# Performance work log

Measured on AMD Instinct MI355X. Metric: run time of the kernel, lower is better.

The kernel has to match this reference:

```python
import jax, jax.numpy as jnp
import numpy as np

D_IN, D_HID, D_OUT = 4096, 8192, 1000


def setup_inputs() -> dict:
    key = jax.random.key(0)
    ks = jax.random.split(key, 7)
    s1 = 1.0 / np.sqrt(D_IN)
    s2 = 1.0 / np.sqrt(D_HID)
    return {
        "x": jax.random.normal(ks[0], (D_IN,), dtype=jnp.float32),
        "W1": jax.random.normal(ks[1], (D_HID, D_IN), dtype=jnp.float32) * s1,
        "b1": jax.random.normal(ks[2], (D_HID,), dtype=jnp.float32) * 0.01,
        "W2": jax.random.normal(ks[3], (D_HID, D_HID), dtype=jnp.float32) * s2,
        "b2": jax.random.normal(ks[4], (D_HID,), dtype=jnp.float32) * 0.01,
        "W3": jax.random.normal(ks[5], (D_OUT, D_HID), dtype=jnp.float32) * s2,
        "b3": jax.random.normal(ks[6], (D_OUT,), dtype=jnp.float32) * 0.01,
    }


def reference(x, W1, b1, W2, b2, W3, b3):
    # layer 1: matvec + bias + square activation (h_relu is x*x)
    h = W1 @ x + b1
    h = h * h
    # layer 2
    h = W2 @ h + b2
    h = h * h
    # layer 3 (no activation)
    return W3 @ h + b3
```

## Files before the change

### kernel.cpp

```cpp
#include <hip/hip_runtime.h>


__global__ __launch_bounds__(256) void init_bias(
    const float* __restrict__ b1, const float* __restrict__ b2,
    const float* __restrict__ b3,
    float* __restrict__ h1, float* __restrict__ h2, float* __restrict__ out)
{
    const int i = blockIdx.x * 256 + threadIdx.x;
    if (i < 8192)       h1[i] = b1[i];
    else if (i < 16384) h2[i - 8192] = b2[i - 8192];
    else if (i < 17384) out[i - 16384] = b3[i - 16384];
}

template<int K, int RPB, int SQ>
__global__ __launch_bounds__(256) void matvec_atomic(
    const float* __restrict__ W,
    const float* __restrict__ xin,
    float* __restrict__ y)
{
    constexpr int K4     = K / 4;
    constexpr int CHUNKS = K4 / 256;

    __shared__ __align__(16) float sx[K];
    const int tid = threadIdx.x;

    const float4* __restrict__ x4 = (const float4*)xin;
    float4* sx4 = (float4*)sx;
    #pragma unroll
    for (int c = 0; c < CHUNKS; ++c) {
        const int i = c * 256 + tid;
        float4 v = x4[i];
        if (SQ) { v.x *= v.x; v.y *= v.y; v.z *= v.z; v.w *= v.w; }
        sx4[i] = v;
    }
    __syncthreads();

    const int  c0   = blockIdx.x % CHUNKS;
    const long row0 = (long)blockIdx.x * RPB;

    for (int r = 0; r < RPB; ++r) {
        const long row = row0 + r;
        const float4* __restrict__ Wr = (const float4*)(W + row * (long)K);

        float acc = 0.0f;
        #pragma unroll
        for (int j = 0; j < CHUNKS; ++j) {
            int c = c0 + j; if (c >= CHUNKS) c -= CHUNKS;
            const int i = c * 256 + tid;
            const float4 w = Wr[i];
            const float4 v = sx4[i];
            acc += (w.x * v.x + w.y * v.y) + (w.z * v.z + w.w * v.w);
        }

        #pragma unroll
        for (int off = 32; off > 0; off >>= 1)
            acc += __shfl_down(acc, off, 64);
        if ((tid & 63) == 0) atomicAdd(&y[row], acc);
    }
}

extern "C" void kernel_launch(void* const* d_in, const int* in_sizes, int n_in,
                              void* d_out, int out_size, void* d_ws, size_t ws_size,
                              hipStream_t stream) {
    const float* x  = (const float*)d_in[0];
    const float* W1 = (const float*)d_in[1];
    const float* b1 = (const float*)d_in[2];
    const float* W2 = (const float*)d_in[3];
    const float* b2 = (const float*)d_in[4];
    const float* W3 = (const float*)d_in[5];
    const float* b3 = (const float*)d_in[6];
    float* out = (float*)d_out;

    float* h1 = (float*)d_ws;
    float* h2 = h1 + 8192;

    init_bias<<<68, 256, 0, stream>>>(b1, b2, b3, h1, h2, out);

    matvec_atomic<4096, 8, 0><<<1024, 256, 0, stream>>>(W1, x, h1);
    matvec_atomic<8192, 8, 1><<<1024, 256, 0, stream>>>(W2, h1, h2);
    matvec_atomic<8192, 2, 1><<<500, 256, 0, stream>>>(W3, h2, out);
}
```

Before: 467.7 us.

## Drop shared-memory staging; process rows jointly with register accumulators and column splits

Replaces the shared-memory staging of the input vector with direct global (cached) loads that are reused across R rows processed together, so several independent weight loads are in flight per thread. Removes the __syncthreads and the 32KB of shared memory per block, which raises the number of resident blocks. Adds a column-segment split (NSEG) for the last layer so it launches more blocks, at the cost of more atomics. The input vector is now reloaded from L2/L1 by each block instead of once into LDS.

```diff
diff --git a/kernel.cpp b/kernel.cpp
--- a/kernel.cpp
+++ b/kernel.cpp
@@ -12,50 +12,53 @@
     else if (i < 17384) out[i - 16384] = b3[i - 16384];
 }
 
-template<int K, int RPB, int SQ>
-__global__ __launch_bounds__(256) void matvec_atomic(
+template<int LDK, int COLS, int R, int NSEG, int SQ>
+__global__ __launch_bounds__(256) void matvec(
     const float* __restrict__ W,
     const float* __restrict__ xin,
     float* __restrict__ y)
 {
-    constexpr int K4     = K / 4;
-    constexpr int CHUNKS = K4 / 256;
+    constexpr int C4     = COLS / 4;
+    constexpr int CHUNKS = C4 / 256;
+    static_assert(CHUNKS * 256 == C4, "COLS must be multiple of 1024");
 
-    __shared__ __align__(16) float sx[K];
-    const int tid = threadIdx.x;
+    const int tid  = threadIdx.x;
+    const int g    = blockIdx.x / NSEG;
+    const int s    = blockIdx.x - g * NSEG;
+    const int row0 = g * R;
 
-    const float4* __restrict__ x4 = (const float4*)xin;
-    float4* sx4 = (float4*)sx;
+    const float4* __restrict__ x4 = (const float4*)(xin + (size_t)s * COLS);
+    const float4* W4[R];
     #pragma unroll
-    for (int c = 0; c < CHUNKS; ++c) {
-        const int i = c * 256 + tid;
+    for (int r = 0; r < R; ++r)
+        W4[r] = (const float4*)(W + (size_t)(row0 + r) * LDK + (size_t)s * COLS);
+
+    float acc[R];
+    #pragma unroll
+    for (int r = 0; r < R; ++r) acc[r] = 0.0f;
+
+    #pragma unroll
+    for (int j = 0; j < CHUNKS; ++j) {
+        const int i = j * 256 + tid;
         float4 v = x4[i];
         if (SQ) { v.x *= v.x; v.y *= v.y; v.z *= v.z; v.w *= v.w; }
-        sx4[i] = v;
+        #pragma unroll
+        for (int r = 0; r < R; ++r) {
+            const float4 w = W4[r][i];
+            acc[r] += (w.x * v.x + w.y * v.y) + (w.z * v.z + w.w * v.w);
+        }
     }
-    __syncthreads();
 
-    const int  c0   = blockIdx.x % CHUNKS;
-    const long row0 = (long)blockIdx.x * RPB;
-
-    for (int r = 0; r < RPB; ++r) {
-        const long row = row0 + r;
-        const float4* __restrict__ Wr = (const float4*)(W + row * (long)K);
-
-        float acc = 0.0f;
+    #pragma unroll
+    for (int off = 32; off > 0; off >>= 1) {
         #pragma unroll
-        for (int j = 0; j < CHUNKS; ++j) {
-            int c = c0 + j; if (c >= CHUNKS) c -= CHUNKS;
-            const int i = c * 256 + tid;
-            const float4 w = Wr[i];
-            const float4 v = sx4[i];
-            acc += (w.x * v.x + w.y * v.y) + (w.z * v.z + w.w * v.w);
-        }
-
+        for (int r = 0; r < R; ++r)
+            acc[r] += __shfl_down(acc[r], off, 64);
+    }
+    if ((tid & 63) == 0) {
         #pragma unroll
-        for (int off = 32; off > 0; off >>= 1)
-            acc += __shfl_down(acc, off, 64);
-        if ((tid & 63) == 0) atomicAdd(&y[row], acc);
+        for (int r = 0; r < R; ++r)
+            atomicAdd(&y[row0 + r], acc[r]);
     }
 }
 
@@ -76,7 +79,7 @@
 
     init_bias<<<68, 256, 0, stream>>>(b1, b2, b3, h1, h2, out);
 
-    matvec_atomic<4096, 8, 0><<<1024, 256, 0, stream>>>(W1, x, h1);
-    matvec_atomic<8192, 8, 1><<<1024, 256, 0, stream>>>(W2, h1, h2);
-    matvec_atomic<8192, 2, 1><<<500, 256, 0, stream>>>(W3, h2, out);
+    matvec<4096, 4096, 4, 1, 0><<<2048, 256, 0, stream>>>(W1, x, h1);
+    matvec<8192, 8192, 4, 1, 1><<<2048, 256, 0, stream>>>(W2, h1, h2);
+    matvec<8192, 2048, 4, 4, 1><<<1000, 256, 0, stream>>>(W3, h2, out);
 }
```

New measurement: 463.8 us. About the same (-0.8%).

## Use one wave per row with nontemporal loads and fold bias init into layers

Applied to the files above, without the earlier changes.

Replaces the block-per-row-group matvec, which staged x in shared memory and accumulated with atomics, with a one-wavefront-per-row design. Each wave reads its row of W with nontemporal loads and reads x straight from global/L2, then writes the result plus bias directly with no atomics. The separate bias-init kernel is removed: layer 2 also initializes the output with b3, and layer 3 splits K into 8 segments across blocks and combines them with atomics. This cuts launches, LDS staging and syncs and adds parallelism, at the cost of every wave re-reading x from cache.

```diff
diff --git a/kernel.cpp b/kernel.cpp
--- a/kernel.cpp
+++ b/kernel.cpp
@@ -1,62 +1,79 @@
 #include <hip/hip_runtime.h>
 
 
-__global__ __launch_bounds__(256) void init_bias(
-    const float* __restrict__ b1, const float* __restrict__ b2,
+typedef float f32x4 __attribute__((ext_vector_type(4)));
+
+template<int K, int SQ, int INIT_OUT>
+__global__ __launch_bounds__(256) void matvec_rowwave(
+    const float* __restrict__ W,
+    const float* __restrict__ xin,
+    const float* __restrict__ bias,
+    float* __restrict__ y,
     const float* __restrict__ b3,
-    float* __restrict__ h1, float* __restrict__ h2, float* __restrict__ out)
+    float* __restrict__ out)
 {
-    const int i = blockIdx.x * 256 + threadIdx.x;
-    if (i < 8192)       h1[i] = b1[i];
-    else if (i < 16384) h2[i - 8192] = b2[i - 8192];
-    else if (i < 17384) out[i - 16384] = b3[i - 16384];
+    constexpr int ITER = K / 4 / 64;
+    const int tid  = threadIdx.x;
+    const int wave = tid >> 6;
+    const int lane = tid & 63;
+    const int row  = blockIdx.x * 4 + wave;
+
+    const f32x4* __restrict__ W4 = (const f32x4*)(W + (size_t)row * K);
+    const f32x4* __restrict__ x4 = (const f32x4*)xin;
+
+    float acc = 0.0f;
+    #pragma unroll 8
+    for (int j = 0; j < ITER; ++j) {
+        const int i = j * 64 + lane;
+        const f32x4 w = __builtin_nontemporal_load(&W4[i]);
+        f32x4 v = x4[i];
+        if (SQ) v *= v;
+        acc += (w.x * v.x + w.y * v.y) + (w.z * v.z + w.w * v.w);
+    }
+
+    #pragma unroll
+    for (int off = 32; off > 0; off >>= 1)
+        acc += __shfl_down(acc, off, 64);
+    if (lane == 0) y[row] = acc + bias[row];
+
+    if (INIT_OUT && blockIdx.x < 4) {
+        const int i = blockIdx.x * 256 + tid;
+        if (i < 1000) out[i] = b3[i];
+    }
 }
 
-template<int K, int RPB, int SQ>
-__global__ __launch_bounds__(256) void matvec_atomic(
+template<int K, int NSEG>
+__global__ __launch_bounds__(256) void matvec_l3(
     const float* __restrict__ W,
     const float* __restrict__ xin,
-    float* __restrict__ y)
+    float* __restrict__ out)
 {
-    constexpr int K4     = K / 4;
-    constexpr int CHUNKS = K4 / 256;
+    constexpr int COLS = K / NSEG;
+    constexpr int ITER = COLS / 4 / 64;
+    const int tid  = threadIdx.x;
+    const int wave = tid >> 6;
+    const int lane = tid & 63;
+    const int g    = blockIdx.x / NSEG;
+    const int s    = blockIdx.x - g * NSEG;
+    const int row  = g * 4 + wave;
 
-    __shared__ __align__(16) float sx[K];
-    const int tid = threadIdx.x;
+    const f32x4* __restrict__ W4 = (const f32x4*)(W + (size_t)row * K + (size_t)s * COLS);
+    const f32x4* __restrict__ x4 = (const f32x4*)(xin + (size_t)s * COLS);
 
-    const float4* __restrict__ x4 = (const float4*)xin;
-    float4* sx4 = (float4*)sx;
+    float acc = 0.0f;
     #pragma unroll
-    for (int c = 0; c < CHUNKS; ++c) {
-        const int i = c * 256 + tid;
-        float4 v = x4[i];
-        if (SQ) { v.x *= v.x; v.y *= v.y; v.z *= v.z; v.w *= v.w; }
-        sx4[i] = v;
+    for (int j = 0; j < ITER; ++j) {
+        const int i = j * 64 + lane;
+        const f32x4 w = __builtin_nontemporal_load(&W4[i]);
+        f32x4 v = x4[i];
+        v *= v;
+        acc += (w.x * v.x + w.y * v.y) + (w.z * v.z + w.w * v.w);
     }
-    __syncthreads();
 
-    const int  c0   = blockIdx.x % CHUNKS;
-    const long row0 = (long)blockIdx.x * RPB;
-
-    for (int r = 0; r < RPB; ++r) {
-        const long row = row0 + r;
-        const float4* __restrict__ Wr = (const float4*)(W + row * (long)K);
-
-        float acc = 0.0f;
-        #pragma unroll
-        for (int j = 0; j < CHUNKS; ++j) {
-            int c = c0 + j; if (c >= CHUNKS) c -= CHUNKS;
-            const int i = c * 256 + tid;
-            const float4 w = Wr[i];
-            const float4 v = sx4[i];
-            acc += (w.x * v.x + w.y * v.y) + (w.z * v.z + w.w * v.w);
-        }
-
-        #pragma unroll
-        for (int off = 32; off > 0; off >>= 1)
-            acc += __shfl_down(acc, off, 64);
-        if ((tid & 63) == 0) atomicAdd(&y[row], acc);
-    }
+    #pragma unroll
+    for (int off = 32; off > 0; off >>= 1)
+        acc += __shfl_down(acc, off, 64);
+    if (lane == 0) atomicAdd(&out[row], acc);
 }
 
 extern "C" void kernel_launch(void* const* d_in, const int* in_sizes, int n_in,
@@ -74,9 +91,7 @@
     float* h1 = (float*)d_ws;
     float* h2 = h1 + 8192;
 
-    init_bias<<<68, 256, 0, stream>>>(b1, b2, b3, h1, h2, out);
-
-    matvec_atomic<4096, 8, 0><<<1024, 256, 0, stream>>>(W1, x, h1);
-    matvec_atomic<8192, 8, 1><<<1024, 256, 0, stream>>>(W2, h1, h2);
-    matvec_atomic<8192, 2, 1><<<500, 256, 0, stream>>>(W3, h2, out);
+    matvec_rowwave<4096, 0, 0><<<2048, 256, 0, stream>>>(W1, x, b1, h1, nullptr, nullptr);
+    matvec_rowwave<8192, 1, 1><<<2048, 256, 0, stream>>>(W2, h1, b2, h2, b3, out);
+    matvec_l3<8192, 8><<<2000, 256, 0, stream>>>(W3, h2, out);
 }
```

Result: faster. 437.3 us (-6.5%).
